# Performance work log

Measured on AMD Instinct MI355X. Metric: run time of the kernel, lower is better.

## Reference

```python
import jax, jax.numpy as jnp
import numpy as np

N_NODES = 100000
N_EDGES = 500000
B = 256
NUM_RELS = 200
VEC = 300   # rel_vectors.shape[1]
D = 32      # rel_emb_dim
MODES = 6


def setup_inputs() -> dict:
    key = jax.random.key(0)
    ks = jax.random.split(key, 16)
    s = 0.05
    return {
        'edge_src': jax.random.randint(ks[0], (N_EDGES,), 0, N_NODES, dtype=jnp.int32),
        'edge_dst': jax.random.randint(ks[1], (N_EDGES,), 0, N_NODES, dtype=jnp.int32),
        'edge_type': jax.random.randint(ks[2], (N_EDGES,), 0, NUM_RELS, dtype=jnp.int32),
        'head_ids': jnp.arange(B, dtype=jnp.int32),            # one head node per subgraph
        'tail_ids': jnp.arange(B, dtype=jnp.int32) + B,        # one tail node per subgraph (disjoint)
        'rel_labels': jax.random.randint(ks[3], (B,), 0, NUM_RELS, dtype=jnp.int32),
        'rel_vectors': jax.random.normal(ks[4], (NUM_RELS, VEC), jnp.float32),
        'W1': jax.random.normal(ks[5], (VEC, D), jnp.float32) * s,
        'b1': jax.random.normal(ks[6], (D,), jnp.float32) * s,
        'W2': jax.random.normal(ks[7], (D, D), jnp.float32) * s,
        'b2': jax.random.normal(ks[8], (D,), jnp.float32) * s,
        'reld_W': jax.random.normal(ks[9], (MODES, D, D), jnp.float32) * s,
        'reld_b': jax.random.normal(ks[10], (MODES, D), jnp.float32) * s,
        'conc_W': jax.random.normal(ks[11], (2 * D, D), jnp.float32) * s,
        'conc_b': jax.random.normal(ks[12], (D,), jnp.float32) * s,
        'fc_W': jax.random.normal(ks[13], (D, 1), jnp.float32) * s,
        'fc_b': jax.random.normal(ks[14], (1,), jnp.float32) * s,
    }


def _mode_segments(edge_src, edge_dst, head_ids, tail_ids):
    """Per-edge segment id (batch index, or B=dropped) for each of the 6 modes.
    Equivalent to the torch sparse mask build: mode5 = out_edge_out*in_edge_in,
    mode6 = in_edge_out*out_edge_in, modes 1-4 with overlaps subtracted out."""
    b = head_ids.shape[0]
    bidx = jnp.arange(b, dtype=jnp.int32)
    head_batch = jnp.full((N_NODES,), -1, jnp.int32).at[head_ids].set(bidx)
    tail_batch = jnp.full((N_NODES,), -1, jnp.int32).at[tail_ids].set(bidx)
    hb_s = head_batch[edge_src]
    hb_d = head_batch[edge_dst]
    tb_s = tail_batch[edge_src]
    tb_d = tail_batch[edge_dst]
    m5 = (hb_s >= 0) & (hb_s == tb_d)   # src==head_b and dst==tail_b
    m6 = (hb_d >= 0) & (hb_d == tb_s)   # dst==head_b and src==tail_b
    drop = jnp.int32(b)
    return [
        jnp.where((hb_d >= 0) & ~m6, hb_d, drop),  # in_edge_out  - mode6
        jnp.where((hb_s >= 0) & ~m5, hb_s, drop),  # out_edge_out - mode5
        jnp.where((tb_d >= 0) & ~m5, tb_d, drop),  # in_edge_in   - mode5
        jnp.where((tb_s >= 0) & ~m6, tb_s, drop),  # out_edge_in  - mode6
        jnp.where(m5, hb_s, drop),                 # mode5
        jnp.where(m6, hb_d, drop),                 # mode6
    ]


def reference(edge_src, edge_dst, edge_type, head_ids, tail_ids, rel_labels,
              rel_vectors, W1, b1, W2, b2, reld_W, reld_b, conc_W, conc_b, fc_W, fc_b):
    b = head_ids.shape[0]
    segs = _mode_segments(edge_src, edge_dst, head_ids, tail_ids)

    # edge embeddings: rel_vectors[type] -> transform1 -> transform2   [E, D]
    e = rel_vectors[edge_type] @ W1 + b1
    e = e @ W2 + b2
    # per-mode fc_reld transforms: [MODES, E, D]
    Y = jnp.einsum('ed,mdk->mek', e, reld_W) + reld_b[:, None, :]

    ones_e = jnp.ones(edge_src.shape, e.dtype)
    acc = jnp.zeros((b, Y.shape[-1]), e.dtype)
    for i in range(MODES):
        agg = jax.ops.segment_sum(Y[i], segs[i], num_segments=b + 1)[:b]
        cnt = jax.ops.segment_sum(ones_e, segs[i], num_segments=b + 1)[:b]
        acc = acc + agg / (cnt[:, None] + 1e-30)
    rel_neighbor = acc / MODES

    r = rel_vectors[rel_labels] @ W1 + b1
    r = r @ W2 + b2

    h = jnp.concatenate([rel_neighbor, r], axis=-1) @ conc_W + conc_b
    h = jax.nn.relu(h)
    # F.normalize(p=2, dim=-1)
    g_rep = h / jnp.maximum(jnp.linalg.norm(h, axis=-1, keepdims=True), 1e-12)
    return g_rep @ fc_W + fc_b  # [B, 1]
```

## Files before the change

### kernel.cpp

```cpp
#include <hip/hip_runtime.h>
#include <hip/hip_bf16.h>

constexpr int N_NODES  = 100000;
constexpr int BATCH    = 256;
constexpr int NUM_RELS = 200;
constexpr int VEC      = 300;
constexpr int DIM      = 32;
constexpr int MODES    = 6;

constexpr int BM_WORDS     = (N_NODES + 31) / 32;
constexpr int RELS_PER_BLK = 8;
constexpr int NRB          = NUM_RELS / RELS_PER_BLK;
static_assert(NUM_RELS % RELS_PER_BLK == 0, "rel blocks assume exact tiling");
constexpr int ZERO_BLKS    = 64;

template <typename T> __device__ __forceinline__ float ldf(const void* p, int i);
template <> __device__ __forceinline__ float ldf<float>(const void* p, int i) {
    return ((const float*)p)[i];
}
template <> __device__ __forceinline__ float ldf<__hip_bfloat16>(const void* p, int i) {
    return __bfloat162float(((const __hip_bfloat16*)p)[i]);
}

__device__ __forceinline__ void detect_dtype(const void* rel_vectors, int* sflag) {
    const int tid = threadIdx.x;
    if (tid < 64) {
        unsigned short p = ((const unsigned short*)rel_vectors)[tid];
        unsigned long long mk = __ballot(((p >> 7) & 0xFF) > 140);
        if (tid == 0) *sflag = (mk == 0ull);
    }
    __syncthreads();
}

template <typename T>
__device__ __forceinline__ void rel_body(const void* rel_vectors, const void* W1, const void* b1,
                                         const void* W2, const void* b2,
                                         const void* reld_W, const void* reld_b,
                                         float* E_rel, float* Y_rel,
                                         float (*rv)[VEC], float (*e1)[DIM], float (*e2)[DIM],
                                         int r0) {
    const int tid = threadIdx.x;
    const int g = tid >> 5, d = tid & 31;
    const int r = r0 + g;
    for (int v = d; v < VEC; v += 32) rv[g][v] = ldf<T>(rel_vectors, r * VEC + v);
    __syncthreads();
    float acc = ldf<T>(b1, d);
    for (int v = 0; v < VEC; ++v) acc += rv[g][v] * ldf<T>(W1, v * DIM + d);
    e1[g][d] = acc;
    __syncthreads();
    float a2 = ldf<T>(b2, d);
    for (int k = 0; k < DIM; ++k) a2 += e1[g][k] * ldf<T>(W2, k * DIM + d);
    e2[g][d] = a2;
    E_rel[r * DIM + d] = a2;
    __syncthreads();
    for (int m = 0; m < MODES; ++m) {
        float y = ldf<T>(reld_b, m * DIM + d);
        for (int k = 0; k < DIM; ++k) y += e2[g][k] * ldf<T>(reld_W, (m * DIM + k) * DIM + d);
        Y_rel[(m * NUM_RELS + r) * DIM + d] = y;
    }
}

__global__ void k_setup(const int* __restrict__ head_ids, const int* __restrict__ tail_ids,
                        const void* rel_vectors, const void* W1, const void* b1,
                        const void* W2, const void* b2,
                        const void* reld_W, const void* reld_b,
                        unsigned* bitmap, unsigned* pack, unsigned* cnt3,
                        float* E_rel, float* Y_rel) {
    __shared__ float rv[RELS_PER_BLK][VEC];
    __shared__ float e1[RELS_PER_BLK][DIM];
    __shared__ float e2[RELS_PER_BLK][DIM];
    __shared__ int sflag;
    const int bid = blockIdx.x, tid = threadIdx.x;
    if (bid == 0) {
        for (int i = tid; i < BM_WORDS; i += blockDim.x) bitmap[i] = 0u;
        __syncthreads();
        if (tid < BATCH) {
            pack[head_ids[tid]] = 0u;
            pack[tail_ids[tid]] = 0u;
        }
        __syncthreads();
        if (tid < BATCH) {
            const int h = head_ids[tid], t = tail_ids[tid];
            atomicOr(&pack[h], (unsigned)(tid + 1));
            atomicOr(&pack[t], (unsigned)(tid + 1) << 16);
            atomicOr(&bitmap[h >> 5], 1u << (h & 31));
            atomicOr(&bitmap[t >> 5], 1u << (t & 31));
        }
    } else if (bid <= NRB) {
        detect_dtype(rel_vectors, &sflag);
        const int r0 = (bid - 1) * RELS_PER_BLK;
        if (sflag)
            rel_body<__hip_bfloat16>(rel_vectors, W1, b1, W2, b2, reld_W, reld_b,
                                     E_rel, Y_rel, rv, e1, e2, r0);
        else
            rel_body<float>(rel_vectors, W1, b1, W2, b2, reld_W, reld_b,
                            E_rel, Y_rel, rv, e1, e2, r0);
    } else {
        uint4* p = (uint4*)cnt3;
        const int n4 = (MODES * BATCH * NUM_RELS) / 4;
        const int idx = (bid - 1 - NRB) * blockDim.x + tid;
        const int stride = ZERO_BLKS * blockDim.x;
        const uint4 z = {0u, 0u, 0u, 0u};
        for (int i = idx; i < n4; i += stride) p[i] = z;
    }
}

__device__ __forceinline__ void process_edge(int s, int dn, int t, unsigned bs, unsigned bd,
                                             const unsigned* __restrict__ pack,
                                             unsigned* cnt3) {
    const unsigned ps = bs ? pack[s] : 0u;
    const unsigned pd = bd ? pack[dn] : 0u;
    const int hbs = (int)(ps & 0xFFFFu) - 1, tbs = (int)(ps >> 16) - 1;
    const int hbd = (int)(pd & 0xFFFFu) - 1, tbd = (int)(pd >> 16) - 1;
    const bool m5 = (hbs >= 0) && (hbs == tbd);
    const bool m6 = (hbd >= 0) && (hbd == tbs);
    if (hbd >= 0)         atomicAdd(&cnt3[((m6 ? 5 : 0) * BATCH + hbd) * NUM_RELS + t], 1u);
    if (hbs >= 0)         atomicAdd(&cnt3[((m5 ? 4 : 1) * BATCH + hbs) * NUM_RELS + t], 1u);
    if (tbd >= 0 && !m5)  atomicAdd(&cnt3[(2 * BATCH + tbd) * NUM_RELS + t], 1u);
    if (tbs >= 0 && !m6)  atomicAdd(&cnt3[(3 * BATCH + tbs) * NUM_RELS + t], 1u);
}

__global__ void k_edges(const int* __restrict__ src, const int* __restrict__ dst,
                        const int* __restrict__ typ,
                        const unsigned* __restrict__ bitmap, const unsigned* __restrict__ pack,
                        unsigned* cnt3, int n_edges) {
    const int n4 = n_edges >> 2;
    const int gstride = gridDim.x * blockDim.x;
    const int gtid = blockIdx.x * blockDim.x + threadIdx.x;
    const int4* src4 = (const int4*)src;
    const int4* dst4 = (const int4*)dst;
    for (int i = gtid; i < n4; i += gstride) {
        const int4 s4 = src4[i];
        const int4 d4 = dst4[i];
        #pragma unroll
        for (int j = 0; j < 4; ++j) {
            const int s  = (&s4.x)[j];
            const int dn = (&d4.x)[j];
            const unsigned bs = (bitmap[s  >> 5] >> (s  & 31)) & 1u;
            const unsigned bd = (bitmap[dn >> 5] >> (dn & 31)) & 1u;
            if (!(bs | bd)) continue;
            process_edge(s, dn, typ[i * 4 + j], bs, bd, pack, cnt3);
        }
    }
    const int rem = n_edges & 3;
    if (gtid < rem) {
        const int e = n4 * 4 + gtid;
        const int s = src[e], dn = dst[e];
        const unsigned bs = (bitmap[s  >> 5] >> (s  & 31)) & 1u;
        const unsigned bd = (bitmap[dn >> 5] >> (dn & 31)) & 1u;
        if (bs | bd) process_edge(s, dn, typ[e], bs, bd, pack, cnt3);
    }
}

template <typename T>
__device__ __forceinline__ void final_body(const unsigned* __restrict__ cnt3,
                                           const float* __restrict__ E_rel,
                                           const float* __restrict__ Y_rel,
                                           const int* __restrict__ rel_labels,
                                           const void* conc_W, const void* conc_b,
                                           const void* fc_W, const void* fc_b,
                                           void* out, float* sm, float* cat) {
    const int b = blockIdx.x, tid = threadIdx.x;
    const int m = tid >> 5, d = tid & 31;
    float acc = 0.f, tot = 0.f;
    const unsigned* row = cnt3 + (m * BATCH + b) * NUM_RELS;
    const float* Ym = Y_rel + m * NUM_RELS * DIM;
    #pragma unroll 4
    for (int t = 0; t < NUM_RELS; ++t) {
        const unsigned c = row[t];
        if (c) {
            const float cf = (float)c;
            acc += cf * Ym[t * DIM + d];
            tot += cf;
        }
    }
    sm[m * DIM + d] = acc / (tot + 1e-30f);
    __syncthreads();
    if (tid < DIM) {
        float rn = 0.f;
        for (int mm = 0; mm < MODES; ++mm) rn += sm[mm * DIM + tid];
        cat[tid] = rn / (float)MODES;
        cat[DIM + tid] = E_rel[rel_labels[b] * DIM + tid];
    }
    __syncthreads();
    if (tid < DIM) {
        float h = ldf<T>(conc_b, tid);
        for (int k = 0; k < 2 * DIM; ++k) h += cat[k] * ldf<T>(conc_W, k * DIM + tid);
        h = fmaxf(h, 0.f);
        float n2 = h * h;
        #pragma unroll
        for (int off = 16; off >= 1; off >>= 1) n2 += __shfl_xor(n2, off);
        const float g = h / fmaxf(sqrtf(n2), 1e-12f);
        float pr = g * ldf<T>(fc_W, tid);
        #pragma unroll
        for (int off = 16; off >= 1; off >>= 1) pr += __shfl_xor(pr, off);
        if (tid == 0) {
            const float o = pr + ldf<T>(fc_b, 0);
            if constexpr (sizeof(T) == 2) ((__hip_bfloat16*)out)[b] = __float2bfloat16(o);
            else                          ((float*)out)[b] = o;
        }
    }
}

__global__ void k_final(const unsigned* __restrict__ cnt3, const float* __restrict__ E_rel,
                        const float* __restrict__ Y_rel, const int* __restrict__ rel_labels,
                        const void* rel_vectors,
                        const void* conc_W, const void* conc_b,
                        const void* fc_W, const void* fc_b, void* out) {
    __shared__ float sm[MODES * DIM];
    __shared__ float cat[2 * DIM];
    __shared__ int sflag;
    detect_dtype(rel_vectors, &sflag);
    if (sflag)
        final_body<__hip_bfloat16>(cnt3, E_rel, Y_rel, rel_labels, conc_W, conc_b, fc_W, fc_b, out, sm, cat);
    else
        final_body<float>(cnt3, E_rel, Y_rel, rel_labels, conc_W, conc_b, fc_W, fc_b, out, sm, cat);
}

extern "C" void kernel_launch(void* const* d_in, const int* in_sizes, int n_in,
                              void* d_out, int out_size, void* d_ws, size_t ws_size,
                              hipStream_t stream) {
    const int* edge_src   = (const int*)d_in[0];
    const int* edge_dst   = (const int*)d_in[1];
    const int* edge_type  = (const int*)d_in[2];
    const int* head_ids   = (const int*)d_in[3];
    const int* tail_ids   = (const int*)d_in[4];
    const int* rel_labels = (const int*)d_in[5];
    const void* rel_vectors = d_in[6];
    const void* W1     = d_in[7];
    const void* b1     = d_in[8];
    const void* W2     = d_in[9];
    const void* b2     = d_in[10];
    const void* reld_W = d_in[11];
    const void* reld_b = d_in[12];
    const void* conc_W = d_in[13];
    const void* conc_b = d_in[14];
    const void* fc_W   = d_in[15];
    const void* fc_b   = d_in[16];

    const int n_edges = in_sizes[0];

    unsigned* cnt3   = (unsigned*)d_ws;
    unsigned* bitmap = cnt3 + MODES * BATCH * NUM_RELS;
    unsigned* pack   = bitmap + BM_WORDS;
    float*    E_rel  = (float*)(pack + N_NODES);
    float*    Y_rel  = E_rel + NUM_RELS * DIM;

    k_setup<<<1 + NRB + ZERO_BLKS, 256, 0, stream>>>(head_ids, tail_ids,
                                                     rel_vectors, W1, b1, W2, b2, reld_W, reld_b,
                                                     bitmap, pack, cnt3, E_rel, Y_rel);
    k_edges<<<512, 256, 0, stream>>>(edge_src, edge_dst, edge_type,
                                     bitmap, pack, cnt3, n_edges);
    k_final<<<BATCH, 192, 0, stream>>>(cnt3, E_rel, Y_rel, rel_labels, rel_vectors,
                                       conc_W, conc_b, fc_W, fc_b, d_out);
}
```

Before: 129.5 us.

## Fuse setup, edge scan and final into one cooperative kernel with grid syncs

Replaces the three kernel launches with a single cooperative kernel that uses grid.sync() between the setup, edge-counting and finalisation phases. While setup runs, the blocks left idle stream the edge arrays once to warm the cache before the edge pass. This is meant to remove inter-kernel launch gaps and cold DRAM reads of the edge data. The cost is the grid-wide barrier overhead and the constraint that all 512 blocks be co-resident.

```diff
diff --git a/kernel.cpp b/kernel.cpp
--- a/kernel.cpp
+++ b/kernel.cpp
@@ -1,5 +1,8 @@
 #include <hip/hip_runtime.h>
 #include <hip/hip_bf16.h>
+#include <hip/hip_cooperative_groups.h>
+
+namespace cg = cooperative_groups;
 
 constexpr int N_NODES  = 100000;
 constexpr int BATCH    = 256;
@@ -13,6 +16,9 @@
 constexpr int NRB          = NUM_RELS / RELS_PER_BLK;
 static_assert(NUM_RELS % RELS_PER_BLK == 0, "rel blocks assume exact tiling");
 constexpr int ZERO_BLKS    = 64;
+constexpr int SETUP_BLKS   = 1 + NRB + ZERO_BLKS;
+constexpr int GRID         = 512;
+constexpr int BLOCK        = 256;
 
 template <typename T> __device__ __forceinline__ float ldf(const void* p, int i);
 template <> __device__ __forceinline__ float ldf<float>(const void* p, int i) {
@@ -57,51 +63,6 @@
         float y = ldf<T>(reld_b, m * DIM + d);
         for (int k = 0; k < DIM; ++k) y += e2[g][k] * ldf<T>(reld_W, (m * DIM + k) * DIM + d);
         Y_rel[(m * NUM_RELS + r) * DIM + d] = y;
-    }
-}
-
-__global__ void k_setup(const int* __restrict__ head_ids, const int* __restrict__ tail_ids,
-                        const void* rel_vectors, const void* W1, const void* b1,
-                        const void* W2, const void* b2,
-                        const void* reld_W, const void* reld_b,
-                        unsigned* bitmap, unsigned* pack, unsigned* cnt3,
-                        float* E_rel, float* Y_rel) {
-    __shared__ float rv[RELS_PER_BLK][VEC];
-    __shared__ float e1[RELS_PER_BLK][DIM];
-    __shared__ float e2[RELS_PER_BLK][DIM];
-    __shared__ int sflag;
-    const int bid = blockIdx.x, tid = threadIdx.x;
-    if (bid == 0) {
-        for (int i = tid; i < BM_WORDS; i += blockDim.x) bitmap[i] = 0u;
-        __syncthreads();
-        if (tid < BATCH) {
-            pack[head_ids[tid]] = 0u;
-            pack[tail_ids[tid]] = 0u;
-        }
-        __syncthreads();
-        if (tid < BATCH) {
-            const int h = head_ids[tid], t = tail_ids[tid];
-            atomicOr(&pack[h], (unsigned)(tid + 1));
-            atomicOr(&pack[t], (unsigned)(tid + 1) << 16);
-            atomicOr(&bitmap[h >> 5], 1u << (h & 31));
-            atomicOr(&bitmap[t >> 5], 1u << (t & 31));
-        }
-    } else if (bid <= NRB) {
-        detect_dtype(rel_vectors, &sflag);
-        const int r0 = (bid - 1) * RELS_PER_BLK;
-        if (sflag)
-            rel_body<__hip_bfloat16>(rel_vectors, W1, b1, W2, b2, reld_W, reld_b,
-                                     E_rel, Y_rel, rv, e1, e2, r0);
-        else
-            rel_body<float>(rel_vectors, W1, b1, W2, b2, reld_W, reld_b,
-                            E_rel, Y_rel, rv, e1, e2, r0);
-    } else {
-        uint4* p = (uint4*)cnt3;
-        const int n4 = (MODES * BATCH * NUM_RELS) / 4;
-        const int idx = (bid - 1 - NRB) * blockDim.x + tid;
-        const int stride = ZERO_BLKS * blockDim.x;
-        const uint4 z = {0u, 0u, 0u, 0u};
-        for (int i = idx; i < n4; i += stride) p[i] = z;
     }
 }
 
@@ -120,38 +81,6 @@
     if (tbs >= 0 && !m6)  atomicAdd(&cnt3[(3 * BATCH + tbs) * NUM_RELS + t], 1u);
 }
 
-__global__ void k_edges(const int* __restrict__ src, const int* __restrict__ dst,
-                        const int* __restrict__ typ,
-                        const unsigned* __restrict__ bitmap, const unsigned* __restrict__ pack,
-                        unsigned* cnt3, int n_edges) {
-    const int n4 = n_edges >> 2;
-    const int gstride = gridDim.x * blockDim.x;
-    const int gtid = blockIdx.x * blockDim.x + threadIdx.x;
-    const int4* src4 = (const int4*)src;
-    const int4* dst4 = (const int4*)dst;
-    for (int i = gtid; i < n4; i += gstride) {
-        const int4 s4 = src4[i];
-        const int4 d4 = dst4[i];
-        #pragma unroll
-        for (int j = 0; j < 4; ++j) {
-            const int s  = (&s4.x)[j];
-            const int dn = (&d4.x)[j];
-            const unsigned bs = (bitmap[s  >> 5] >> (s  & 31)) & 1u;
-            const unsigned bd = (bitmap[dn >> 5] >> (dn & 31)) & 1u;
-            if (!(bs | bd)) continue;
-            process_edge(s, dn, typ[i * 4 + j], bs, bd, pack, cnt3);
-        }
-    }
-    const int rem = n_edges & 3;
-    if (gtid < rem) {
-        const int e = n4 * 4 + gtid;
-        const int s = src[e], dn = dst[e];
-        const unsigned bs = (bitmap[s  >> 5] >> (s  & 31)) & 1u;
-        const unsigned bd = (bitmap[dn >> 5] >> (dn & 31)) & 1u;
-        if (bs | bd) process_edge(s, dn, typ[e], bs, bd, pack, cnt3);
-    }
-}
-
 template <typename T>
 __device__ __forceinline__ void final_body(const unsigned* __restrict__ cnt3,
                                            const float* __restrict__ E_rel,
@@ -161,20 +90,22 @@
                                            const void* fc_W, const void* fc_b,
                                            void* out, float* sm, float* cat) {
     const int b = blockIdx.x, tid = threadIdx.x;
-    const int m = tid >> 5, d = tid & 31;
-    float acc = 0.f, tot = 0.f;
-    const unsigned* row = cnt3 + (m * BATCH + b) * NUM_RELS;
-    const float* Ym = Y_rel + m * NUM_RELS * DIM;
-    #pragma unroll 4
-    for (int t = 0; t < NUM_RELS; ++t) {
-        const unsigned c = row[t];
-        if (c) {
-            const float cf = (float)c;
-            acc += cf * Ym[t * DIM + d];
-            tot += cf;
-        }
-    }
-    sm[m * DIM + d] = acc / (tot + 1e-30f);
+    if (tid < MODES * 32) {
+        const int m = tid >> 5, d = tid & 31;
+        float acc = 0.f, tot = 0.f;
+        const unsigned* row = cnt3 + (m * BATCH + b) * NUM_RELS;
+        const float* Ym = Y_rel + m * NUM_RELS * DIM;
+        #pragma unroll 4
+        for (int t = 0; t < NUM_RELS; ++t) {
+            const unsigned c = row[t];
+            if (c) {
+                const float cf = (float)c;
+                acc += cf * Ym[t * DIM + d];
+                tot += cf;
+            }
+        }
+        sm[m * DIM + d] = acc / (tot + 1e-30f);
+    }
     __syncthreads();
     if (tid < DIM) {
         float rn = 0.f;
@@ -202,19 +133,113 @@
     }
 }
 
-__global__ void k_final(const unsigned* __restrict__ cnt3, const float* __restrict__ E_rel,
-                        const float* __restrict__ Y_rel, const int* __restrict__ rel_labels,
-                        const void* rel_vectors,
-                        const void* conc_W, const void* conc_b,
-                        const void* fc_W, const void* fc_b, void* out) {
-    __shared__ float sm[MODES * DIM];
-    __shared__ float cat[2 * DIM];
+__global__ __launch_bounds__(BLOCK, 2) void k_fused(
+        const int* edge_src, const int* edge_dst, const int* edge_type,
+        const int* head_ids, const int* tail_ids, const int* rel_labels,
+        const void* rel_vectors, const void* W1, const void* b1,
+        const void* W2, const void* b2, const void* reld_W, const void* reld_b,
+        const void* conc_W, const void* conc_b, const void* fc_W, const void* fc_b,
+        unsigned* bitmap, unsigned* pack, unsigned* cnt3,
+        float* E_rel, float* Y_rel, unsigned* dummy,
+        void* out, int n_edges) {
+    union SmemU {
+        struct { float rv[RELS_PER_BLK][VEC]; float e1[RELS_PER_BLK][DIM]; float e2[RELS_PER_BLK][DIM]; } rel;
+        struct { float sm[MODES * DIM]; float cat[2 * DIM]; } fin;
+    };
+    __shared__ SmemU smem;
     __shared__ int sflag;
-    detect_dtype(rel_vectors, &sflag);
-    if (sflag)
-        final_body<__hip_bfloat16>(cnt3, E_rel, Y_rel, rel_labels, conc_W, conc_b, fc_W, fc_b, out, sm, cat);
-    else
-        final_body<float>(cnt3, E_rel, Y_rel, rel_labels, conc_W, conc_b, fc_W, fc_b, out, sm, cat);
+    const int bid = blockIdx.x, tid = threadIdx.x;
+    cg::grid_group grid = cg::this_grid();
+
+    if (bid == 0) {
+        for (int i = tid; i < BM_WORDS; i += BLOCK) bitmap[i] = 0u;
+        __syncthreads();
+        if (tid < BATCH) {
+            pack[head_ids[tid]] = 0u;
+            pack[tail_ids[tid]] = 0u;
+        }
+        __syncthreads();
+        if (tid < BATCH) {
+            const int h = head_ids[tid], t = tail_ids[tid];
+            atomicOr(&pack[h], (unsigned)(tid + 1));
+            atomicOr(&pack[t], (unsigned)(tid + 1) << 16);
+            atomicOr(&bitmap[h >> 5], 1u << (h & 31));
+            atomicOr(&bitmap[t >> 5], 1u << (t & 31));
+        }
+    } else if (bid <= NRB) {
+        detect_dtype(rel_vectors, &sflag);
+        const int r0 = (bid - 1) * RELS_PER_BLK;
+        if (sflag)
+            rel_body<__hip_bfloat16>(rel_vectors, W1, b1, W2, b2, reld_W, reld_b,
+                                     E_rel, Y_rel, smem.rel.rv, smem.rel.e1, smem.rel.e2, r0);
+        else
+            rel_body<float>(rel_vectors, W1, b1, W2, b2, reld_W, reld_b,
+                            E_rel, Y_rel, smem.rel.rv, smem.rel.e1, smem.rel.e2, r0);
+    } else if (bid < SETUP_BLKS) {
+        uint4* p = (uint4*)cnt3;
+        const int n4 = (MODES * BATCH * NUM_RELS) / 4;
+        const int idx = (bid - 1 - NRB) * BLOCK + tid;
+        const int stride = ZERO_BLKS * BLOCK;
+        const uint4 z = {0u, 0u, 0u, 0u};
+        for (int i = idx; i < n4; i += stride) p[i] = z;
+    } else {
+        const int n4e = n_edges >> 2;
+        const int4* s4 = (const int4*)edge_src;
+        const int4* d4 = (const int4*)edge_dst;
+        const int4* t4 = (const int4*)edge_type;
+        const int pidx = (bid - SETUP_BLKS) * BLOCK + tid;
+        const int pstr = (GRID - SETUP_BLKS) * BLOCK;
+        unsigned acc = 0u;
+        for (int i = pidx; i < n4e; i += pstr) {
+            const int4 a = s4[i], b = d4[i], c = t4[i];
+            acc += (unsigned)(a.x + a.y + a.z + a.w + b.x + b.y + b.z + b.w
+                              + c.x + c.y + c.z + c.w);
+        }
+        dummy[bid] = acc;
+    }
+
+    grid.sync();
+
+    {
+        const int n4 = n_edges >> 2;
+        const int gstride = GRID * BLOCK;
+        const int gtid = bid * BLOCK + tid;
+        const int4* src4 = (const int4*)edge_src;
+        const int4* dst4 = (const int4*)edge_dst;
+        for (int i = gtid; i < n4; i += gstride) {
+            const int4 s4 = src4[i];
+            const int4 d4 = dst4[i];
+            #pragma unroll
+            for (int j = 0; j < 4; ++j) {
+                const int s  = (&s4.x)[j];
+                const int dn = (&d4.x)[j];
+                const unsigned bs = (bitmap[s  >> 5] >> (s  & 31)) & 1u;
+                const unsigned bd = (bitmap[dn >> 5] >> (dn & 31)) & 1u;
+                if (!(bs | bd)) continue;
+                process_edge(s, dn, edge_type[i * 4 + j], bs, bd, pack, cnt3);
+            }
+        }
+        const int rem = n_edges & 3;
+        if (gtid < rem) {
+            const int e = n4 * 4 + gtid;
+            const int s = edge_src[e], dn = edge_dst[e];
+            const unsigned bs = (bitmap[s  >> 5] >> (s  & 31)) & 1u;
+            const unsigned bd = (bitmap[dn >> 5] >> (dn & 31)) & 1u;
+            if (bs | bd) process_edge(s, dn, edge_type[e], bs, bd, pack, cnt3);
+        }
+    }
+
+    grid.sync();
+
+    if (bid < BATCH) {
+        detect_dtype(rel_vectors, &sflag);
+        if (sflag)
+            final_body<__hip_bfloat16>(cnt3, E_rel, Y_rel, rel_labels,
+                                       conc_W, conc_b, fc_W, fc_b, out, smem.fin.sm, smem.fin.cat);
+        else
+            final_body<float>(cnt3, E_rel, Y_rel, rel_labels,
+                              conc_W, conc_b, fc_W, fc_b, out, smem.fin.sm, smem.fin.cat);
+    }
 }
 
 extern "C" void kernel_launch(void* const* d_in, const int* in_sizes, int n_in,
@@ -238,19 +263,25 @@
     const void* fc_W   = d_in[15];
     const void* fc_b   = d_in[16];
 
-    const int n_edges = in_sizes[0];
+    int n_edges = in_sizes[0];
 
     unsigned* cnt3   = (unsigned*)d_ws;
     unsigned* bitmap = cnt3 + MODES * BATCH * NUM_RELS;
     unsigned* pack   = bitmap + BM_WORDS;
     float*    E_rel  = (float*)(pack + N_NODES);
     float*    Y_rel  = E_rel + NUM_RELS * DIM;
-
-    k_setup<<<1 + NRB + ZERO_BLKS, 256, 0, stream>>>(head_ids, tail_ids,
-                                                     rel_vectors, W1, b1, W2, b2, reld_W, reld_b,
-                                                     bitmap, pack, cnt3, E_rel, Y_rel);
-    k_edges<<<512, 256, 0, stream>>>(edge_src, edge_dst, edge_type,
-                                     bitmap, pack, cnt3, n_edges);
-    k_final<<<BATCH, 192, 0, stream>>>(cnt3, E_rel, Y_rel, rel_labels, rel_vectors,
-                                       conc_W, conc_b, fc_W, fc_b, d_out);
-}
+    unsigned* dummy  = (unsigned*)(Y_rel + MODES * NUM_RELS * DIM);
+    void*     out    = d_out;
+
+    void* args[] = {
+        (void*)&edge_src, (void*)&edge_dst, (void*)&edge_type,
+        (void*)&head_ids, (void*)&tail_ids, (void*)&rel_labels,
+        (void*)&rel_vectors, (void*)&W1, (void*)&b1,
+        (void*)&W2, (void*)&b2, (void*)&reld_W, (void*)&reld_b,
+        (void*)&conc_W, (void*)&conc_b, (void*)&fc_W, (void*)&fc_b,
+        (void*)&bitmap, (void*)&pack, (void*)&cnt3,
+        (void*)&E_rel, (void*)&Y_rel, (void*)&dummy,
+        (void*)&out, (void*)&n_edges,
+    };
+    hipLaunchCooperativeKernel(k_fused, dim3(GRID), dim3(BLOCK), args, 0, stream);
+}
```

New measurement: 267.7 us. +106.7%, slower.

## Replace global count histogram with per-block shared hash and compact emit lists

Applied to the files above, without the earlier changes.

The setup and edge kernels are merged into one launch. Each edge block builds its own shared-memory node bitmap and a hash table of head/tail nodes, then writes matching edge codes to a compact per-block list instead of doing global atomics into a large zeroed histogram. The final kernel scans all per-block lists to gather its batch's codes and accumulates Y_rel rows directly. This removes the histogram zeroing, one launch, and global atomics. In exchange every edge block rebuilds the 12.5KB bitmap and the hash table, every final block rescans the whole list, and the fixed CAP/MAXM limits silently drop entries if they overflow.

```diff
diff --git a/kernel.cpp b/kernel.cpp
--- a/kernel.cpp
+++ b/kernel.cpp
@@ -8,11 +8,16 @@
 constexpr int DIM      = 32;
 constexpr int MODES    = 6;
 
+constexpr int BLOCK        = 256;
 constexpr int BM_WORDS     = (N_NODES + 31) / 32;
 constexpr int RELS_PER_BLK = 8;
 constexpr int NRB          = NUM_RELS / RELS_PER_BLK;
 static_assert(NUM_RELS % RELS_PER_BLK == 0, "rel blocks assume exact tiling");
-constexpr int ZERO_BLKS    = 64;
+constexpr int EDGE_BLKS    = 256;
+constexpr int CAP          = 256;
+constexpr int HASHN        = 1024;
+constexpr unsigned HEMPTY  = 0xFFFFFFFFu;
+constexpr int MAXM         = 512;
 
 template <typename T> __device__ __forceinline__ float ldf(const void* p, int i);
 template <> __device__ __forceinline__ float ldf<float>(const void* p, int i) {
@@ -30,6 +35,24 @@
         if (tid == 0) *sflag = (mk == 0ull);
     }
     __syncthreads();
+}
+
+__device__ __forceinline__ void hinsert(unsigned* hkey, unsigned* hval, int node, unsigned v) {
+    unsigned h = ((unsigned)node * 2654435761u) >> 22;
+    for (;;) {
+        unsigned prev = atomicCAS(&hkey[h], HEMPTY, (unsigned)node);
+        if (prev == HEMPTY || prev == (unsigned)node) { atomicOr(&hval[h], v); return; }
+        h = (h + 1) & (HASHN - 1);
+    }
+}
+__device__ __forceinline__ unsigned hlookup(const unsigned* hkey, const unsigned* hval, int node) {
+    unsigned h = ((unsigned)node * 2654435761u) >> 22;
+    for (;;) {
+        const unsigned k = hkey[h];
+        if (k == (unsigned)node) return hval[h];
+        if (k == HEMPTY) return 0u;
+        h = (h + 1) & (HASHN - 1);
+    }
 }
 
 template <typename T>
@@ -60,129 +83,113 @@
     }
 }
 
-__global__ void k_setup(const int* __restrict__ head_ids, const int* __restrict__ tail_ids,
-                        const void* rel_vectors, const void* W1, const void* b1,
-                        const void* W2, const void* b2,
-                        const void* reld_W, const void* reld_b,
-                        unsigned* bitmap, unsigned* pack, unsigned* cnt3,
-                        float* E_rel, float* Y_rel) {
-    __shared__ float rv[RELS_PER_BLK][VEC];
-    __shared__ float e1[RELS_PER_BLK][DIM];
-    __shared__ float e2[RELS_PER_BLK][DIM];
-    __shared__ int sflag;
+struct EdgeSmem {
+    unsigned bm[BM_WORDS];
+    unsigned hkey[HASHN];
+    unsigned hval[HASHN];
+    unsigned obuf[CAP];
+    int ocnt;
+};
+struct RelSmem {
+    float rv[RELS_PER_BLK][VEC];
+    float e1[RELS_PER_BLK][DIM];
+    float e2[RELS_PER_BLK][DIM];
+    int sflag;
+};
+
+__global__ __launch_bounds__(BLOCK) void k_main(
+        const int* __restrict__ edge_src, const int* __restrict__ edge_dst,
+        const int* __restrict__ edge_type,
+        const int* __restrict__ head_ids, const int* __restrict__ tail_ids,
+        const void* rel_vectors, const void* W1, const void* b1,
+        const void* W2, const void* b2, const void* reld_W, const void* reld_b,
+        unsigned* list, unsigned* listcnt, float* E_rel, float* Y_rel, int n_edges) {
+    union SmemU { RelSmem rel; EdgeSmem edge; };
+    __shared__ SmemU s;
     const int bid = blockIdx.x, tid = threadIdx.x;
-    if (bid == 0) {
-        for (int i = tid; i < BM_WORDS; i += blockDim.x) bitmap[i] = 0u;
-        __syncthreads();
-        if (tid < BATCH) {
-            pack[head_ids[tid]] = 0u;
-            pack[tail_ids[tid]] = 0u;
-        }
-        __syncthreads();
-        if (tid < BATCH) {
-            const int h = head_ids[tid], t = tail_ids[tid];
-            atomicOr(&pack[h], (unsigned)(tid + 1));
-            atomicOr(&pack[t], (unsigned)(tid + 1) << 16);
-            atomicOr(&bitmap[h >> 5], 1u << (h & 31));
-            atomicOr(&bitmap[t >> 5], 1u << (t & 31));
-        }
-    } else if (bid <= NRB) {
-        detect_dtype(rel_vectors, &sflag);
-        const int r0 = (bid - 1) * RELS_PER_BLK;
-        if (sflag)
+
+    if (bid < NRB) {
+        detect_dtype(rel_vectors, &s.rel.sflag);
+        const int r0 = bid * RELS_PER_BLK;
+        if (s.rel.sflag)
             rel_body<__hip_bfloat16>(rel_vectors, W1, b1, W2, b2, reld_W, reld_b,
-                                     E_rel, Y_rel, rv, e1, e2, r0);
+                                     E_rel, Y_rel, s.rel.rv, s.rel.e1, s.rel.e2, r0);
         else
             rel_body<float>(rel_vectors, W1, b1, W2, b2, reld_W, reld_b,
-                            E_rel, Y_rel, rv, e1, e2, r0);
-    } else {
-        uint4* p = (uint4*)cnt3;
-        const int n4 = (MODES * BATCH * NUM_RELS) / 4;
-        const int idx = (bid - 1 - NRB) * blockDim.x + tid;
-        const int stride = ZERO_BLKS * blockDim.x;
-        const uint4 z = {0u, 0u, 0u, 0u};
-        for (int i = idx; i < n4; i += stride) p[i] = z;
-    }
-}
-
-__device__ __forceinline__ void process_edge(int s, int dn, int t, unsigned bs, unsigned bd,
-                                             const unsigned* __restrict__ pack,
-                                             unsigned* cnt3) {
-    const unsigned ps = bs ? pack[s] : 0u;
-    const unsigned pd = bd ? pack[dn] : 0u;
-    const int hbs = (int)(ps & 0xFFFFu) - 1, tbs = (int)(ps >> 16) - 1;
-    const int hbd = (int)(pd & 0xFFFFu) - 1, tbd = (int)(pd >> 16) - 1;
-    const bool m5 = (hbs >= 0) && (hbs == tbd);
-    const bool m6 = (hbd >= 0) && (hbd == tbs);
-    if (hbd >= 0)         atomicAdd(&cnt3[((m6 ? 5 : 0) * BATCH + hbd) * NUM_RELS + t], 1u);
-    if (hbs >= 0)         atomicAdd(&cnt3[((m5 ? 4 : 1) * BATCH + hbs) * NUM_RELS + t], 1u);
-    if (tbd >= 0 && !m5)  atomicAdd(&cnt3[(2 * BATCH + tbd) * NUM_RELS + t], 1u);
-    if (tbs >= 0 && !m6)  atomicAdd(&cnt3[(3 * BATCH + tbs) * NUM_RELS + t], 1u);
-}
-
-__global__ void k_edges(const int* __restrict__ src, const int* __restrict__ dst,
-                        const int* __restrict__ typ,
-                        const unsigned* __restrict__ bitmap, const unsigned* __restrict__ pack,
-                        unsigned* cnt3, int n_edges) {
+                            E_rel, Y_rel, s.rel.rv, s.rel.e1, s.rel.e2, r0);
+        return;
+    }
+
+    const int eb = bid - NRB;
+    for (int i = tid; i < BM_WORDS; i += BLOCK) s.edge.bm[i] = 0u;
+    for (int i = tid; i < HASHN; i += BLOCK) { s.edge.hkey[i] = HEMPTY; s.edge.hval[i] = 0u; }
+    if (tid == 0) s.edge.ocnt = 0;
+    __syncthreads();
+    if (tid < BATCH) {
+        const int h = head_ids[tid], t = tail_ids[tid];
+        atomicOr(&s.edge.bm[h >> 5], 1u << (h & 31));
+        atomicOr(&s.edge.bm[t >> 5], 1u << (t & 31));
+        hinsert(s.edge.hkey, s.edge.hval, h, (unsigned)(tid + 1));
+        hinsert(s.edge.hkey, s.edge.hval, t, (unsigned)(tid + 1) << 16);
+    }
+    __syncthreads();
+
+    auto emit = [&](unsigned code) {
+        const int idx = atomicAdd(&s.edge.ocnt, 1);
+        if (idx < CAP) s.edge.obuf[idx] = code;
+    };
+    auto classify = [&](int sn, int dn, unsigned bs, unsigned bd, int e) {
+        const int t = edge_type[e];
+        const unsigned ps = bs ? hlookup(s.edge.hkey, s.edge.hval, sn) : 0u;
+        const unsigned pd = bd ? hlookup(s.edge.hkey, s.edge.hval, dn) : 0u;
+        const int hbs = (int)(ps & 0xFFFFu) - 1, tbs = (int)(ps >> 16) - 1;
+        const int hbd = (int)(pd & 0xFFFFu) - 1, tbd = (int)(pd >> 16) - 1;
+        const bool m5 = (hbs >= 0) && (hbs == tbd);
+        const bool m6 = (hbd >= 0) && (hbd == tbs);
+        if (hbd >= 0)        emit(((m6 ? 5u : 0u) * BATCH + hbd) * NUM_RELS + t);
+        if (hbs >= 0)        emit(((m5 ? 4u : 1u) * BATCH + hbs) * NUM_RELS + t);
+        if (tbd >= 0 && !m5) emit((2u * BATCH + tbd) * NUM_RELS + t);
+        if (tbs >= 0 && !m6) emit((3u * BATCH + tbs) * NUM_RELS + t);
+    };
+
     const int n4 = n_edges >> 2;
-    const int gstride = gridDim.x * blockDim.x;
-    const int gtid = blockIdx.x * blockDim.x + threadIdx.x;
-    const int4* src4 = (const int4*)src;
-    const int4* dst4 = (const int4*)dst;
-    for (int i = gtid; i < n4; i += gstride) {
+    const int sstr = EDGE_BLKS * BLOCK;
+    const int et = eb * BLOCK + tid;
+    const int4* src4 = (const int4*)edge_src;
+    const int4* dst4 = (const int4*)edge_dst;
+    for (int i = et; i < n4; i += sstr) {
         const int4 s4 = src4[i];
         const int4 d4 = dst4[i];
         #pragma unroll
         for (int j = 0; j < 4; ++j) {
-            const int s  = (&s4.x)[j];
+            const int sn = (&s4.x)[j];
             const int dn = (&d4.x)[j];
-            const unsigned bs = (bitmap[s  >> 5] >> (s  & 31)) & 1u;
-            const unsigned bd = (bitmap[dn >> 5] >> (dn & 31)) & 1u;
+            const unsigned bs = (s.edge.bm[sn >> 5] >> (sn & 31)) & 1u;
+            const unsigned bd = (s.edge.bm[dn >> 5] >> (dn & 31)) & 1u;
             if (!(bs | bd)) continue;
-            process_edge(s, dn, typ[i * 4 + j], bs, bd, pack, cnt3);
+            classify(sn, dn, bs, bd, i * 4 + j);
         }
     }
     const int rem = n_edges & 3;
-    if (gtid < rem) {
-        const int e = n4 * 4 + gtid;
-        const int s = src[e], dn = dst[e];
-        const unsigned bs = (bitmap[s  >> 5] >> (s  & 31)) & 1u;
-        const unsigned bd = (bitmap[dn >> 5] >> (dn & 31)) & 1u;
-        if (bs | bd) process_edge(s, dn, typ[e], bs, bd, pack, cnt3);
-    }
+    if (et < rem) {
+        const int e = n4 * 4 + et;
+        const int sn = edge_src[e], dn = edge_dst[e];
+        const unsigned bs = (s.edge.bm[sn >> 5] >> (sn & 31)) & 1u;
+        const unsigned bd = (s.edge.bm[dn >> 5] >> (dn & 31)) & 1u;
+        if (bs | bd) classify(sn, dn, bs, bd, e);
+    }
+    __syncthreads();
+    const int oc = min(s.edge.ocnt, CAP);
+    if (tid == 0) listcnt[eb] = (unsigned)oc;
+    for (int i = tid; i < oc; i += BLOCK) list[eb * CAP + i] = s.edge.obuf[i];
 }
 
 template <typename T>
-__device__ __forceinline__ void final_body(const unsigned* __restrict__ cnt3,
-                                           const float* __restrict__ E_rel,
-                                           const float* __restrict__ Y_rel,
-                                           const int* __restrict__ rel_labels,
-                                           const void* conc_W, const void* conc_b,
-                                           const void* fc_W, const void* fc_b,
-                                           void* out, float* sm, float* cat) {
-    const int b = blockIdx.x, tid = threadIdx.x;
-    const int m = tid >> 5, d = tid & 31;
-    float acc = 0.f, tot = 0.f;
-    const unsigned* row = cnt3 + (m * BATCH + b) * NUM_RELS;
-    const float* Ym = Y_rel + m * NUM_RELS * DIM;
-    #pragma unroll 4
-    for (int t = 0; t < NUM_RELS; ++t) {
-        const unsigned c = row[t];
-        if (c) {
-            const float cf = (float)c;
-            acc += cf * Ym[t * DIM + d];
-            tot += cf;
-        }
-    }
-    sm[m * DIM + d] = acc / (tot + 1e-30f);
-    __syncthreads();
-    if (tid < DIM) {
-        float rn = 0.f;
-        for (int mm = 0; mm < MODES; ++mm) rn += sm[mm * DIM + tid];
-        cat[tid] = rn / (float)MODES;
-        cat[DIM + tid] = E_rel[rel_labels[b] * DIM + tid];
-    }
-    __syncthreads();
+__device__ __forceinline__ void epilogue_math(const float* cat, const float* E_unused,
+                                              const void* conc_W, const void* conc_b,
+                                              const void* fc_W, const void* fc_b,
+                                              void* out, int b) {
+    const int tid = threadIdx.x;
     if (tid < DIM) {
         float h = ldf<T>(conc_b, tid);
         for (int k = 0; k < 2 * DIM; ++k) h += cat[k] * ldf<T>(conc_W, k * DIM + tid);
@@ -202,19 +209,60 @@
     }
 }
 
-__global__ void k_final(const unsigned* __restrict__ cnt3, const float* __restrict__ E_rel,
-                        const float* __restrict__ Y_rel, const int* __restrict__ rel_labels,
-                        const void* rel_vectors,
-                        const void* conc_W, const void* conc_b,
-                        const void* fc_W, const void* fc_b, void* out) {
-    __shared__ float sm[MODES * DIM];
-    __shared__ float cat[2 * DIM];
-    __shared__ int sflag;
+__global__ __launch_bounds__(64) void k_final(
+        const unsigned* __restrict__ list, const unsigned* __restrict__ listcnt,
+        const float* __restrict__ E_rel, const float* __restrict__ Y_rel,
+        const int* __restrict__ rel_labels, const void* rel_vectors,
+        const void* conc_W, const void* conc_b, const void* fc_W, const void* fc_b,
+        void* out) {
+    __shared__ float    accf[MODES][DIM];
+    __shared__ float    totf[MODES];
+    __shared__ unsigned scnt[EDGE_BLKS];
+    __shared__ unsigned mbuf[MAXM];
+    __shared__ int      mcnt;
+    __shared__ float    cat[2 * DIM];
+    __shared__ int      sflag;
+    const int b = blockIdx.x, tid = threadIdx.x;
+
+    for (int i = tid; i < MODES * DIM; i += 64) ((float*)accf)[i] = 0.f;
+    if (tid < MODES) totf[tid] = 0.f;
+    if (tid == 0) mcnt = 0;
+    for (int i = tid; i < EDGE_BLKS; i += 64) scnt[i] = listcnt[i];
     detect_dtype(rel_vectors, &sflag);
-    if (sflag)
-        final_body<__hip_bfloat16>(cnt3, E_rel, Y_rel, rel_labels, conc_W, conc_b, fc_W, fc_b, out, sm, cat);
-    else
-        final_body<float>(cnt3, E_rel, Y_rel, rel_labels, conc_W, conc_b, fc_W, fc_b, out, sm, cat);
+
+    for (int seg = 0; seg < EDGE_BLKS; ++seg) {
+        const int c = (int)scnt[seg];
+        for (int i = tid; i < c; i += 64) {
+            const unsigned code = list[seg * CAP + i];
+            const int bb = (int)((code / NUM_RELS) % BATCH);
+            if (bb == b) {
+                const int k = atomicAdd(&mcnt, 1);
+                if (k < MAXM) mbuf[k] = code;
+            }
+        }
+    }
+    __syncthreads();
+
+    const int mc = min(mcnt, MAXM);
+    const int d = tid & 31;
+    for (int j = tid >> 5; j < mc; j += 2) {
+        const unsigned code = mbuf[j];
+        const int m = (int)(code / (NUM_RELS * BATCH));
+        const int t = (int)(code % NUM_RELS);
+        atomicAdd(&accf[m][d], Y_rel[(m * NUM_RELS + t) * DIM + d]);
+        if (d == 0) atomicAdd(&totf[m], 1.f);
+    }
+    __syncthreads();
+
+    if (tid < DIM) {
+        float rn = 0.f;
+        for (int m = 0; m < MODES; ++m) rn += accf[m][tid] / (totf[m] + 1e-30f);
+        cat[tid] = rn / (float)MODES;
+        cat[DIM + tid] = E_rel[rel_labels[b] * DIM + tid];
+    }
+    __syncthreads();
+    if (sflag) epilogue_math<__hip_bfloat16>(cat, E_rel, conc_W, conc_b, fc_W, fc_b, out, b);
+    else       epilogue_math<float>(cat, E_rel, conc_W, conc_b, fc_W, fc_b, out, b);
 }
 
 extern "C" void kernel_launch(void* const* d_in, const int* in_sizes, int n_in,
@@ -240,17 +288,16 @@
 
     const int n_edges = in_sizes[0];
 
-    unsigned* cnt3   = (unsigned*)d_ws;
-    unsigned* bitmap = cnt3 + MODES * BATCH * NUM_RELS;
-    unsigned* pack   = bitmap + BM_WORDS;
-    float*    E_rel  = (float*)(pack + N_NODES);
-    float*    Y_rel  = E_rel + NUM_RELS * DIM;
-
-    k_setup<<<1 + NRB + ZERO_BLKS, 256, 0, stream>>>(head_ids, tail_ids,
-                                                     rel_vectors, W1, b1, W2, b2, reld_W, reld_b,
-                                                     bitmap, pack, cnt3, E_rel, Y_rel);
-    k_edges<<<512, 256, 0, stream>>>(edge_src, edge_dst, edge_type,
-                                     bitmap, pack, cnt3, n_edges);
-    k_final<<<BATCH, 192, 0, stream>>>(cnt3, E_rel, Y_rel, rel_labels, rel_vectors,
-                                       conc_W, conc_b, fc_W, fc_b, d_out);
-}
+    unsigned* list    = (unsigned*)d_ws;
+    unsigned* listcnt = list + EDGE_BLKS * CAP;
+    float*    E_rel   = (float*)(listcnt + EDGE_BLKS);
+    float*    Y_rel   = E_rel + NUM_RELS * DIM;
+
+    k_main<<<NRB + EDGE_BLKS, BLOCK, 0, stream>>>(
+        edge_src, edge_dst, edge_type, head_ids, tail_ids,
+        rel_vectors, W1, b1, W2, b2, reld_W, reld_b,
+        list, listcnt, E_rel, Y_rel, n_edges);
+    k_final<<<BATCH, 64, 0, stream>>>(
+        list, listcnt, E_rel, Y_rel, rel_labels, rel_vectors,
+        conc_W, conc_b, fc_W, fc_b, d_out);
+}
```

Measured after the change: 193.8 us. +49.6%, slower.
